# Kernel optimization log

Measured on AMD Instinct MI355X. Metric: run time of the kernel, lower is better.

## Reference

```python
import jax, jax.numpy as jnp
import numpy as np
from jax import lax

B, H, W = 256, 28, 28
LATENT = 64
SOM = (16, 16)
FLAT = 7 * 7 * 256  # encoder feature size after two 2x2 pools


def conv2d_same(x, w, b):
    # x: NHWC, w: HWIO
    return lax.conv_general_dilated(x, w, (1, 1), 'SAME',
                                    dimension_numbers=('NHWC', 'HWIO', 'NHWC')) + b


def maxpool_2x2(x):
    return lax.reduce_window(x, -jnp.inf, lax.max, (1, 2, 2, 1), (1, 2, 2, 1), 'SAME')


def upsample_2x(x):
    return jnp.repeat(jnp.repeat(x, 2, axis=1), 2, axis=2)


def encode(x, conv1_w, conv1_b, conv2_w, conv2_b, enc_w, enc_b):
    h = jax.nn.relu(conv2d_same(x, conv1_w, conv1_b))      # [B,28,28,256]
    h = maxpool_2x2(h)                                      # [B,14,14,256]
    h = jax.nn.relu(conv2d_same(h, conv2_w, conv2_b))      # [B,14,14,256]
    h = maxpool_2x2(h)                                      # [B,7,7,256]
    h = h.reshape(h.shape[0], -1)                           # [B,12544]
    return h @ enc_w + enc_b                                # [B,latent]


def decode(z, dec_w, dec_b, deconv1_w, deconv1_b, deconv2_w, deconv2_b):
    h = z @ dec_w + dec_b                                   # [B,12544]
    h = h.reshape(-1, 7, 7, 256)
    h = upsample_2x(h)                                      # [B,14,14,256]
    h = jax.nn.relu(conv2d_same(h, deconv1_w, deconv1_b))
    h = upsample_2x(h)                                      # [B,28,28,256]
    h = conv2d_same(h, deconv2_w, deconv2_b)                # [B,28,28,1]
    return jax.nn.sigmoid(h)


def setup_inputs() -> dict:
    key = jax.random.key(0)
    ks = jax.random.split(key, 12)
    tn = lambda k, shp, s: jax.random.truncated_normal(k, -2.0, 2.0, shp, jnp.float32) * s
    return {
        'x': jax.random.uniform(ks[0], (B, H, W, 1), jnp.float32),
        'conv1_w': tn(ks[1], (4, 4, 1, 256), 0.1),
        'conv1_b': jnp.full((256,), 0.1, jnp.float32),
        'conv2_w': tn(ks[2], (4, 4, 256, 256), 0.1),
        'conv2_b': jnp.full((256,), 0.1, jnp.float32),
        'enc_w': tn(ks[3], (FLAT, LATENT), 0.02),
        'enc_b': jnp.zeros((LATENT,), jnp.float32),
        'embeddings': tn(ks[4], (SOM[0], SOM[1], LATENT), 0.05),
        'dec_w': tn(ks[5], (LATENT, FLAT), 0.02),
        'dec_b': jnp.zeros((FLAT,), jnp.float32),
        'deconv1_w': tn(ks[6], (4, 4, 256, 256), 0.1),
        'deconv1_b': jnp.full((256,), 0.1, jnp.float32),
        'deconv2_w': tn(ks[7], (4, 4, 256, 1), 0.1),
        'deconv2_b': jnp.full((1,), 0.1, jnp.float32),
    }


def reference(x, conv1_w, conv1_b, conv2_w, conv2_b, enc_w, enc_b, embeddings,
              dec_w, dec_b, deconv1_w, deconv1_b, deconv2_w, deconv2_b):
    z_e = encode(x, conv1_w, conv1_b, conv2_w, conv2_b, enc_w, enc_b)  # [B,D]
    emb_flat = embeddings.reshape(-1, LATENT)                          # [K,D]
    # squared euclidean distances [B,K] (cdist pattern)
    z_dist_flat = jnp.sum(jnp.square(z_e[:, None, :] - emb_flat[None, :, :]), axis=-1)
    k = jnp.argmin(z_dist_flat, axis=-1)                               # [B]
    z_q = emb_flat[k]                                                  # [B,D]
    x_hat_e = decode(z_e, dec_w, dec_b, deconv1_w, deconv1_b, deconv2_w, deconv2_b)
    x_hat_q = decode(z_q, dec_w, dec_b, deconv1_w, deconv1_b, deconv2_w, deconv2_b)
    return jnp.stack([x_hat_e, x_hat_q], axis=0)  # [2,B,28,28,1]
```

## Files before the change

kernel.cpp:

```cpp
#include <hip/hip_runtime.h>
#include <hip/hip_bf16.h>

typedef unsigned short u16;
using short8 = __attribute__((ext_vector_type(8))) short;
using half8  = __attribute__((ext_vector_type(8))) _Float16;
using half4  = __attribute__((ext_vector_type(4))) _Float16;
using half2v = __attribute__((ext_vector_type(2))) _Float16;
using f32x4  = __attribute__((ext_vector_type(4))) float;

__device__ __forceinline__ u16 f2bf(float f) {
    unsigned int u = __float_as_uint(f);
    u += 0x7FFFu + ((u >> 16) & 1u);
    return (u16)(u >> 16);
}
__device__ __forceinline__ float bf2f(u16 h) {
    return __uint_as_float(((unsigned int)h) << 16);
}

__device__ __forceinline__ void gl_lds16(const void* g, void* l) {
    __builtin_amdgcn_global_load_lds((const __attribute__((address_space(1))) void*)g,
                                     (__attribute__((address_space(3))) void*)l, 16, 0, 0);
}

#define PIPE_WAIT8() asm volatile("s_waitcnt vmcnt(8)" ::: "memory")
#define PIPE_WAIT0() asm volatile("s_waitcnt vmcnt(0)" ::: "memory")
#define BAR() __builtin_amdgcn_s_barrier()

__global__ __launch_bounds__(256) void wprep_split_kernel(const float* __restrict__ src,
                                                          u16* __restrict__ hi, u16* __restrict__ lo) {
    int idx = blockIdx.x * 256 + threadIdx.x;
    int ci = idx & 255, n = (idx >> 8) & 255, kk = idx >> 16;
    float v = src[(kk * 256 + ci) * 256 + n];
    u16 h = f2bf(v);
    hi[idx] = h;
    lo[idx] = f2bf(v - bf2f(h));
}

__global__ __launch_bounds__(256) void wprep_dc1_par(const float* __restrict__ src, _Float16* __restrict__ dst) {
    const int idx = blockIdx.x * 256 + threadIdx.x;
    const int ci = idx & 255, n = (idx >> 8) & 255, tg = idx >> 16;
    int p, j;
    if (tg < 9)       { p = 0; j = tg; }
    else if (tg < 15) { p = 1; j = tg - 9; }
    else if (tg < 21) { p = 2; j = tg - 15; }
    else              { p = 3; j = tg - 21; }
    const int dy = p >> 1, dx = p & 1;
    const int nx = 3 - dx;
    const int oyi = j / nx, oxi = j % nx;
    int ky0, kyn, kx0, kxn;
    if (dy == 0) { ky0 = (oyi == 0) ? 0 : (oyi == 1 ? 1 : 3); kyn = (oyi == 1) ? 2 : 1; }
    else         { ky0 = (oyi == 0) ? 0 : 2;                  kyn = 2; }
    if (dx == 0) { kx0 = (oxi == 0) ? 0 : (oxi == 1 ? 1 : 3); kxn = (oxi == 1) ? 2 : 1; }
    else         { kx0 = (oxi == 0) ? 0 : 2;                  kxn = 2; }
    float s = 0.f;
    for (int a = 0; a < kyn; ++a)
        for (int c = 0; c < kxn; ++c)
            s += src[(((ky0 + a) * 4 + (kx0 + c)) * 256 + ci) * 256 + n];
    dst[((size_t)tg << 16) + (n << 8) + ci] = (_Float16)s;
}

__global__ __launch_bounds__(256) void wprep_dc2_par(const float* __restrict__ src, _Float16* __restrict__ dst) {
    const int idx = blockIdx.x * 256 + threadIdx.x;
    if (idx >= 9216) return;
    const int ci = idx & 255;
    const int j9 = (idx >> 8) % 9, p = (idx >> 8) / 9;
    const int dy = p >> 1, dx = p & 1;
    const int oyi = j9 / 3, oxi = j9 % 3;
    float s = 0.f;
    if (!((dy == 1 && oyi == 2) || (dx == 1 && oxi == 2))) {
        int ky0, kyn, kx0, kxn;
        if (dy == 0) { ky0 = (oyi == 0) ? 0 : (oyi == 1 ? 1 : 3); kyn = (oyi == 1) ? 2 : 1; }
        else         { ky0 = (oyi == 0) ? 0 : 2;                  kyn = 2; }
        if (dx == 0) { kx0 = (oxi == 0) ? 0 : (oxi == 1 ? 1 : 3); kxn = (oxi == 1) ? 2 : 1; }
        else         { kx0 = (oxi == 0) ? 0 : 2;                  kxn = 2; }
        for (int a = 0; a < kyn; ++a)
            for (int c = 0; c < kxn; ++c)
                s += src[((ky0 + a) * 4 + (kx0 + c)) * 256 + ci];
    }
    dst[idx] = (_Float16)s;
}

__global__ __launch_bounds__(256) void conv1_pool_v2(const float* __restrict__ x,
                                                     const float* __restrict__ w,
                                                     const float* __restrict__ bias,
                                                     u16* __restrict__ hi, u16* __restrict__ lo) {
    __shared__ float xs[5][32];
    const int blk = blockIdx.x;
    const int py = blk % 14, b = blk / 14;
    const int t = threadIdx.x;
    for (int i = t; i < 160; i += 256) {
        const int r = i >> 5, c = i & 31;
        const int gy = 2 * py - 1 + r, gx = c - 1;
        float v = 0.f;
        if ((unsigned)gy < 28u && (unsigned)gx < 28u) v = x[(b * 28 + gy) * 28 + gx];
        xs[r][c] = v;
    }
    __syncthreads();
    float wr[16];
#pragma unroll
    for (int k = 0; k < 16; ++k) wr[k] = w[k * 256 + t];
    const float bs = bias[t];
    for (int px = 0; px < 14; ++px) {
        float m = 0.f;
#pragma unroll
        for (int dy = 0; dy < 2; ++dy)
#pragma unroll
            for (int dx = 0; dx < 2; ++dx) {
                float a = bs;
#pragma unroll
                for (int ky = 0; ky < 4; ++ky)
#pragma unroll
                    for (int kx = 0; kx < 4; ++kx)
                        a += xs[dy + ky][2 * px + dx + kx] * wr[ky * 4 + kx];
                m = fmaxf(m, a);
            }
        u16 h = f2bf(m);
        const int o = ((b * 14 + py) * 14 + px) * 256 + t;
        hi[o] = h;
        lo[o] = f2bf(m - bf2f(h));
    }
}

__global__ __launch_bounds__(256, 2) void conv2_split_v3(const u16* __restrict__ Ih, const u16* __restrict__ Il,
                                                         const u16* __restrict__ Wh, const u16* __restrict__ Wl,
                                                         const u16* __restrict__ zg,
                                                         const float* __restrict__ bias, float* __restrict__ out) {
    __shared__ __align__(16) short lds[32768];
    const int t = threadIdx.x, lane = t & 63, w = t >> 6;
    const int wm = w >> 1, wn = w & 1;
    const int l16 = lane & 15, l4 = lane >> 4;
    const int m0 = blockIdx.x * 128, n0 = blockIdx.y * 128;

    const int rl8 = lane >> 3;
    const int g = (lane & 7) ^ rl8;
    const u16* selA = (g < 4 ? Ih : Il) + ((g & 3) << 3);
    const u16* selB = (g < 4 ? Wh : Wl) + ((g & 3) << 3);

    int ay[4], ax[4], ab[4], wb[4];
#pragma unroll
    for (int j = 0; j < 4; ++j) {
        const int r = w * 32 + j * 8 + rl8;
        const int gm = m0 + r;
        const int b = gm / 196, rem = gm % 196;
        ay[j] = rem / 14; ax[j] = rem % 14; ab[j] = b * 196;
        wb[j] = (n0 + r) << 8;
    }
    int aoff[4]; bool av[4];
    auto dectap = [&](int kk) {
        const int ky = kk >> 2, kx = kk & 3;
#pragma unroll
        for (int j = 0; j < 4; ++j) {
            const int iy = ay[j] + ky - 1, ix = ax[j] + kx - 1;
            av[j] = ((unsigned)iy < 14u) && ((unsigned)ix < 14u);
            aoff[j] = (ab[j] + iy * 14 + ix) << 8;
        }
    };
    int rdA[4], rdB[4];
#pragma unroll
    for (int mi = 0; mi < 4; ++mi) {
        const int ra = wm * 64 + mi * 16 + l16;
        rdA[mi] = (ra << 6) + ((l4 ^ (ra & 7)) << 3);
    }
#pragma unroll
    for (int ni = 0; ni < 4; ++ni) {
        const int rb = wn * 64 + ni * 16 + l16;
        rdB[ni] = 8192 + (rb << 6) + ((l4 ^ (rb & 7)) << 3);
    }
    auto stage = [&](int h) {
        const int kk = h >> 3, kc = (h & 7) << 5;
        const int buf = (h & 1) << 14;
#pragma unroll
        for (int j = 0; j < 4; ++j) {
            const int rowb = buf + ((w * 32 + j * 8) << 6);
            const u16* asrc = av[j] ? (selA + aoff[j] + kc) : zg;
            gl_lds16(asrc, lds + rowb);
            gl_lds16(selB + (kk << 16) + wb[j] + kc, lds + 8192 + rowb);
        }
    };

    f32x4 acc[4][4] = {};
    dectap(0);
    stage(0);
    for (int h = 0; h < 128; ++h) {
        const int hn = (h < 127) ? h + 1 : 127;
        if ((hn & 7) == 0) dectap(hn >> 3);
        stage(hn);
        PIPE_WAIT8();
        BAR();
        const int base = (h & 1) << 14;
        short8 bh8[4], bl8[4];
#pragma unroll
        for (int ni = 0; ni < 4; ++ni) {
            bh8[ni] = *(const short8*)&lds[base + rdB[ni]];
            bl8[ni] = *(const short8*)&lds[base + (rdB[ni] ^ 32)];
        }
#pragma unroll
        for (int mi = 0; mi < 4; ++mi) {
            const short8 ah = *(const short8*)&lds[base + rdA[mi]];
            const short8 al = *(const short8*)&lds[base + (rdA[mi] ^ 32)];
#pragma unroll
            for (int ni = 0; ni < 4; ++ni) {
                acc[mi][ni] = __builtin_amdgcn_mfma_f32_16x16x32_bf16(ah, bh8[ni], acc[mi][ni], 0, 0, 0);
                acc[mi][ni] = __builtin_amdgcn_mfma_f32_16x16x32_bf16(ah, bl8[ni], acc[mi][ni], 0, 0, 0);
                acc[mi][ni] = __builtin_amdgcn_mfma_f32_16x16x32_bf16(al, bh8[ni], acc[mi][ni], 0, 0, 0);
            }
        }
        BAR();
    }
    PIPE_WAIT0();
#pragma unroll
    for (int ni = 0; ni < 4; ++ni) {
        const int col = n0 + wn * 64 + ni * 16 + l16;
        const float bv = bias[col];
#pragma unroll
        for (int mi = 0; mi < 4; ++mi) {
            const int mrow = m0 + wm * 64 + mi * 16 + l4 * 4;
#pragma unroll
            for (int r = 0; r < 4; ++r)
                out[(size_t)(mrow + r) * 256 + col] = fmaxf(acc[mi][ni][r] + bv, 0.f);
        }
    }
}

__global__ __launch_bounds__(256, 2) void deconv1_par(const _Float16* __restrict__ I,
                                                      const _Float16* __restrict__ WC,
                                                      const _Float16* __restrict__ zg,
                                                      const float* __restrict__ bias,
                                                      _Float16* __restrict__ out) {
    __shared__ __align__(16) _Float16 lds[32768];
    const int t = threadIdx.x, lane = t & 63, w = t >> 6;
    const int wm = w >> 1, wn = w & 1;
    const int l16 = lane & 15, l4 = lane >> 4;
    const int m0 = blockIdx.x * 128, n0 = blockIdx.y * 128;
    const int p = blockIdx.z, dy = p >> 1, dx = p & 1;
    const int nx = 3 - dx;
    const int ntaps = (3 - dy) * nx;
    const int pbase = (dy == 0) ? (dx == 0 ? 0 : 9) : (dx == 0 ? 15 : 21);
    const int nkt = ntaps * 4;

    const int rl8 = lane >> 3;
    const int g = (lane & 7) ^ rl8;
    const _Float16* selA = I + (g << 3);
    const _Float16* selB = WC + ((size_t)pbase << 16) + (g << 3);

    int aY[4], aX[4], ab[4], wb[4];
#pragma unroll
    for (int j = 0; j < 4; ++j) {
        const int r = w * 32 + j * 8 + rl8;
        const int gm = m0 + r;
        const int b = gm / 49, rem = gm % 49;
        aY[j] = rem / 7; aX[j] = rem % 7; ab[j] = b * 49;
        wb[j] = (n0 + r) << 8;
    }
    int aoff[4]; bool av[4];
    auto dectap = [&](int kk) {
        const int oy = kk / nx - (dy == 0 ? 1 : 0);
        const int ox = kk % nx - (dx == 0 ? 1 : 0);
#pragma unroll
        for (int j = 0; j < 4; ++j) {
            const int iy = aY[j] + oy, ix = aX[j] + ox;
            av[j] = ((unsigned)iy < 7u) && ((unsigned)ix < 7u);
            aoff[j] = (ab[j] + iy * 7 + ix) << 8;
        }
    };
    int rdA[4], rdB[4];
#pragma unroll
    for (int mi = 0; mi < 4; ++mi) {
        const int ra = wm * 64 + mi * 16 + l16;
        rdA[mi] = (ra << 6) + ((l4 ^ (ra & 7)) << 3);
    }
#pragma unroll
    for (int ni = 0; ni < 4; ++ni) {
        const int rb = wn * 64 + ni * 16 + l16;
        rdB[ni] = 8192 + (rb << 6) + ((l4 ^ (rb & 7)) << 3);
    }
    auto stage = [&](int kt) {
        const int kk = kt >> 2, kc = (kt & 3) << 6;
        const int buf = (kt & 1) << 14;
#pragma unroll
        for (int j = 0; j < 4; ++j) {
            const int rowb = buf + ((w * 32 + j * 8) << 6);
            const _Float16* asrc = av[j] ? (selA + aoff[j] + kc) : zg;
            gl_lds16(asrc, lds + rowb);
            gl_lds16(selB + (kk << 16) + wb[j] + kc, lds + 8192 + rowb);
        }
    };

    f32x4 acc[4][4] = {};
    dectap(0);
    stage(0);
    for (int kt = 0; kt < nkt; ++kt) {
        const int ktn = (kt < nkt - 1) ? kt + 1 : kt;
        if ((ktn & 3) == 0 && ktn == kt + 1) dectap(ktn >> 2);
        stage(ktn);
        PIPE_WAIT8();
        BAR();
        const int base = (kt & 1) << 14;
#pragma unroll
        for (int ks = 0; ks < 2; ++ks) {
            const int x32 = ks << 5;
            half8 b8[4];
#pragma unroll
            for (int ni = 0; ni < 4; ++ni)
                b8[ni] = *(const half8*)&lds[base + (rdB[ni] ^ x32)];
#pragma unroll
            for (int mi = 0; mi < 4; ++mi) {
                const half8 a8 = *(const half8*)&lds[base + (rdA[mi] ^ x32)];
#pragma unroll
                for (int ni = 0; ni < 4; ++ni)
                    acc[mi][ni] = __builtin_amdgcn_mfma_f32_16x16x32_f16(a8, b8[ni], acc[mi][ni], 0, 0, 0);
            }
        }
        BAR();
    }
    PIPE_WAIT0();
#pragma unroll
    for (int mi = 0; mi < 4; ++mi) {
        const int mb = m0 + wm * 64 + mi * 16 + l4 * 4;
#pragma unroll
        for (int r = 0; r < 4; ++r) {
            const int m = mb + r;
            const int b = m / 49, rem = m % 49;
            const int Y = rem / 7, X = rem % 7;
            _Float16* op = out + (((size_t)(b * 196 + (2 * Y + dy) * 14 + (2 * X + dx))) << 8);
#pragma unroll
            for (int ni = 0; ni < 4; ++ni) {
                const int col = n0 + wn * 64 + ni * 16 + l16;
                op[col] = (_Float16)fmaxf(acc[mi][ni][r] + bias[col], 0.f);
            }
        }
    }
}

__global__ __launch_bounds__(256) void pool2_kernel(const float* __restrict__ h2, float* __restrict__ h2p) {
    int idx = blockIdx.x * 256 + threadIdx.x;
    int c = idx & 255;
    int rest = idx >> 8;
    int px = rest % 7, py = (rest / 7) % 7, b = rest / 49;
    const float* base = h2 + (((size_t)(b * 14 + 2 * py)) * 14 + 2 * px) * 256 + c;
    float v = fmaxf(fmaxf(base[0], base[256]), fmaxf(base[14 * 256], base[14 * 256 + 256]));
    h2p[idx] = v;
}

__global__ __launch_bounds__(256) void enc_kernel(const float* __restrict__ h2p, const float* __restrict__ ew,
                                                  const float* __restrict__ eb, float* __restrict__ zcat) {
    __shared__ float arow[12544];
    __shared__ float part[256];
    const int b = blockIdx.x, t = threadIdx.x;
    const float* src = h2p + (size_t)b * 12544;
    for (int i = t; i < 12544; i += 256) arow[i] = src[i];
    __syncthreads();
    const int n = t & 63, chunk = t >> 6;
    float acc = 0.f;
    const int k0 = chunk * 3136;
    for (int k = k0; k < k0 + 3136; ++k) acc += arow[k] * ew[k * 64 + n];
    part[t] = acc;
    __syncthreads();
    if (t < 64) zcat[b * 64 + t] = part[t] + part[t + 64] + part[t + 128] + part[t + 192] + eb[t];
}

__global__ __launch_bounds__(256) void som_kernel(const float* __restrict__ emb, float* __restrict__ zcat) {
    __shared__ float zrow[64];
    __shared__ float sd[256];
    __shared__ int si[256];
    const int b = blockIdx.x, t = threadIdx.x;
    if (t < 64) zrow[t] = zcat[b * 64 + t];
    __syncthreads();
    float acc = 0.f;
    const float* e = emb + t * 64;
    for (int d = 0; d < 64; ++d) { float df = zrow[d] - e[d]; acc += df * df; }
    sd[t] = acc; si[t] = t;
    __syncthreads();
    for (int off = 128; off >= 1; off >>= 1) {
        if (t < off) {
            float d2 = sd[t + off]; int i2 = si[t + off];
            if (d2 < sd[t] || (d2 == sd[t] && i2 < si[t])) { sd[t] = d2; si[t] = i2; }
        }
        __syncthreads();
    }
    const int k = si[0];
    if (t < 64) zcat[(256 + b) * 64 + t] = emb[k * 64 + t];
}

__global__ __launch_bounds__(256) void dec_kernel(const float* __restrict__ zcat, const float* __restrict__ dw,
                                                  const float* __restrict__ db, _Float16* __restrict__ dech) {
    __shared__ float z[8][64];
    const int t = threadIdx.x;
    const int bg = blockIdx.x / 49;
    const int nc = blockIdx.x % 49;
    for (int i = t; i < 512; i += 256) z[i >> 6][i & 63] = zcat[bg * 512 + i];
    __syncthreads();
    const int n = nc * 256 + t;
    const float bv = db[n];
    float acc[8];
#pragma unroll
    for (int j = 0; j < 8; ++j) acc[j] = bv;
    for (int k = 0; k < 64; ++k) {
        float wv = dw[(size_t)k * 12544 + n];
#pragma unroll
        for (int j = 0; j < 8; ++j) acc[j] += z[j][k] * wv;
    }
#pragma unroll
    for (int j = 0; j < 8; ++j) dech[((size_t)(bg * 8 + j)) * 12544 + n] = (_Float16)acc[j];
}

__global__ __launch_bounds__(256) void deconv2_v3(const _Float16* __restrict__ d1, const _Float16* __restrict__ w2c,
                                                  const float* __restrict__ bias, float* __restrict__ out) {
    __shared__ _Float16 ds[6400];
    __shared__ _Float16 wl[9216];
    const int t = threadIdx.x;
    const int blk = blockIdx.x;
    const int tile = blk % 49, b = blk / 49;
    const int ty = tile / 7, tx = tile % 7;
    const int iy0 = 2 * ty - 1, ix0 = 2 * tx - 1;
    for (int i = t; i < 2304; i += 256)
        *(half4*)&wl[i * 4] = *(const half4*)&w2c[i * 4];
    const half4 z4 = {};
    for (int i = t; i < 1600; i += 256) {
        const int pix = i >> 6, c4 = (i & 63) << 2;
        const int py = pix / 5, px = pix % 5;
        const int iy = iy0 + py, ix = ix0 + px;
        half4 v = z4;
        if ((unsigned)iy < 14u && (unsigned)ix < 14u)
            v = *(const half4*)&d1[(((size_t)(b * 14 + iy)) * 14 + ix) * 256 + c4];
        *(half4*)&ds[pix * 256 + c4] = v;
    }
    __syncthreads();
    const int wv = t >> 6, lane = t & 63;
    const int ci0 = lane * 4;
    const float bv = bias[0];
#pragma unroll
    for (int pp = 0; pp < 4; ++pp) {
        const int pq = wv + pp * 4;
        const int oy = ty * 4 + (pq >> 2), ox = tx * 4 + (pq & 3);
        const int dy = oy & 1, Y = oy >> 1;
        const int dxp = ox & 1, X = ox >> 1;
        const _Float16* wbase = wl + ((dy * 2 + dxp) * 9) * 256 + ci0;
        float acc = 0.f;
#pragma unroll
        for (int j = 0; j < 9; ++j) {
            const int oyi = j / 3, oxi = j % 3;
            const int iy = Y + oyi - (dy == 0 ? 1 : 0);
            const int ix = X + oxi - (dxp == 0 ? 1 : 0);
            const int lp = (iy - iy0) * 5 + (ix - ix0);
            const half4 dv = *(const half4*)&ds[lp * 256 + ci0];
            const half4 wv4 = *(const half4*)&wbase[j * 256];
            half2v dlo = {dv.x, dv.y}, dhi = {dv.z, dv.w};
            half2v wlo = {wv4.x, wv4.y}, whi = {wv4.z, wv4.w};
            acc = __builtin_amdgcn_fdot2(dlo, wlo, acc, false);
            acc = __builtin_amdgcn_fdot2(dhi, whi, acc, false);
        }
#pragma unroll
        for (int off = 32; off; off >>= 1) acc += __shfl_xor(acc, off);
        if (lane == 0) out[(size_t)b * 784 + oy * 28 + ox] = 1.f / (1.f + expf(-(acc + bv)));
    }
}

extern "C" void kernel_launch(void* const* d_in, const int* in_sizes, int n_in,
                              void* d_out, int out_size, void* d_ws, size_t ws_size,
                              hipStream_t stream) {
    const float* x    = (const float*)d_in[0];
    const float* c1w  = (const float*)d_in[1];
    const float* c1b  = (const float*)d_in[2];
    const float* c2w  = (const float*)d_in[3];
    const float* c2b  = (const float*)d_in[4];
    const float* ew   = (const float*)d_in[5];
    const float* eb   = (const float*)d_in[6];
    const float* emb  = (const float*)d_in[7];
    const float* dw   = (const float*)d_in[8];
    const float* db   = (const float*)d_in[9];
    const float* dc1w = (const float*)d_in[10];
    const float* dc1b = (const float*)d_in[11];
    const float* dc2w = (const float*)d_in[12];
    const float* dc2b = (const float*)d_in[13];
    float* out = (float*)d_out;

    char* ws = (char*)d_ws;
    size_t off = 0;
    auto alloc = [&](size_t bytes) { size_t o = off; off += (bytes + 255) & ~(size_t)255; return o; };

    u16*      h1p_hi = (u16*)(ws + alloc((size_t)256 * 196 * 256 * 2));
    u16*      h1p_lo = (u16*)(ws + alloc((size_t)256 * 196 * 256 * 2));
    u16*      w2T_hi = (u16*)(ws + alloc((size_t)16 * 256 * 256 * 2));
    u16*      w2T_lo = (u16*)(ws + alloc((size_t)16 * 256 * 256 * 2));
    float*    h2     = (float*)(ws + alloc((size_t)256 * 196 * 256 * 4));
    float*    h2p    = (float*)(ws + alloc((size_t)256 * 49 * 256 * 4));
    float*    zcat   = (float*)(ws + alloc((size_t)512 * 64 * 4));
    _Float16* dech   = (_Float16*)(ws + alloc((size_t)512 * 49 * 256 * 2));
    _Float16* wc1    = (_Float16*)(ws + alloc((size_t)25 * 256 * 256 * 2));
    _Float16* d1     = (_Float16*)(ws + alloc((size_t)512 * 196 * 256 * 2));
    _Float16* w2c    = (_Float16*)(ws + alloc((size_t)9216 * 2));
    u16*      zg     = (u16*)(ws + alloc(256));

    hipMemsetAsync(zg, 0, 256, stream);
    wprep_split_kernel<<<4096, 256, 0, stream>>>(c2w, w2T_hi, w2T_lo);
    wprep_dc1_par<<<6400, 256, 0, stream>>>(dc1w, wc1);
    wprep_dc2_par<<<36, 256, 0, stream>>>(dc2w, w2c);
    conv1_pool_v2<<<3584, 256, 0, stream>>>(x, c1w, c1b, h1p_hi, h1p_lo);
    conv2_split_v3<<<dim3(392, 2), 256, 0, stream>>>(h1p_hi, h1p_lo, w2T_hi, w2T_lo, zg, c2b, h2);
    pool2_kernel<<<12544, 256, 0, stream>>>(h2, h2p);
    enc_kernel<<<256, 256, 0, stream>>>(h2p, ew, eb, zcat);
    som_kernel<<<256, 256, 0, stream>>>(emb, zcat);
    dec_kernel<<<3136, 256, 0, stream>>>(zcat, dw, db, dech);
    deconv1_par<<<dim3(196, 2, 4), 256, 0, stream>>>(dech, wc1, (const _Float16*)zg, dc1b, d1);
    deconv2_v3<<<25088, 256, 0, stream>>>(d1, w2c, dc2b, out);
}
```

Before: 841.0 us.

## Switch conv GEMMs to 32x32 MFMA, split encoder matmul, retile deconv2

Conv2 and deconv1 move from 16x16x32 MFMA tiles to 32x32x16 tiles with 2x2 accumulators per wave. This cuts the number of LDS fragment reads per MFMA and changes the epilogue store pattern. The encoder dense layer becomes a split-K partial kernel over 98 chunks plus a reduction kernel, reusing the h2 buffer for the partials. Deconv2 now processes row bands per block, keeps its weights in registers and uses far fewer blocks, at the cost of more registers and a serial per-pixel loop.

```diff
diff --git a/kernel.cpp b/kernel.cpp
--- a/kernel.cpp
+++ b/kernel.cpp
@@ -7,6 +7,7 @@
 using half4  = __attribute__((ext_vector_type(4))) _Float16;
 using half2v = __attribute__((ext_vector_type(2))) _Float16;
 using f32x4  = __attribute__((ext_vector_type(4))) float;
+using f32x16 = __attribute__((ext_vector_type(16))) float;
 
 __device__ __forceinline__ u16 f2bf(float f) {
     unsigned int u = __float_as_uint(f);
@@ -121,14 +122,14 @@
     }
 }
 
-__global__ __launch_bounds__(256, 2) void conv2_split_v3(const u16* __restrict__ Ih, const u16* __restrict__ Il,
+__global__ __launch_bounds__(256, 2) void conv2_split_v4(const u16* __restrict__ Ih, const u16* __restrict__ Il,
                                                          const u16* __restrict__ Wh, const u16* __restrict__ Wl,
                                                          const u16* __restrict__ zg,
                                                          const float* __restrict__ bias, float* __restrict__ out) {
     __shared__ __align__(16) short lds[32768];
     const int t = threadIdx.x, lane = t & 63, w = t >> 6;
     const int wm = w >> 1, wn = w & 1;
-    const int l16 = lane & 15, l4 = lane >> 4;
+    const int l32 = lane & 31, lh = lane >> 5;
     const int m0 = blockIdx.x * 128, n0 = blockIdx.y * 128;
 
     const int rl8 = lane >> 3;
@@ -155,16 +156,24 @@
             aoff[j] = (ab[j] + iy * 14 + ix) << 8;
         }
     };
-    int rdA[4], rdB[4];
-#pragma unroll
-    for (int mi = 0; mi < 4; ++mi) {
-        const int ra = wm * 64 + mi * 16 + l16;
-        rdA[mi] = (ra << 6) + ((l4 ^ (ra & 7)) << 3);
-    }
-#pragma unroll
-    for (int ni = 0; ni < 4; ++ni) {
-        const int rb = wn * 64 + ni * 16 + l16;
-        rdB[ni] = 8192 + (rb << 6) + ((l4 ^ (rb & 7)) << 3);
+    int offA[2][2], offB[2][2];
+#pragma unroll
+    for (int mi = 0; mi < 2; ++mi) {
+        const int row = wm * 64 + mi * 32 + l32;
+#pragma unroll
+        for (int ks = 0; ks < 2; ++ks) {
+            const int c = ks * 2 + lh;
+            offA[mi][ks] = (row << 6) + ((c ^ (row & 7)) << 3);
+        }
+    }
+#pragma unroll
+    for (int ni = 0; ni < 2; ++ni) {
+        const int row = wn * 64 + ni * 32 + l32;
+#pragma unroll
+        for (int ks = 0; ks < 2; ++ks) {
+            const int c = ks * 2 + lh;
+            offB[ni][ks] = 8192 + (row << 6) + ((c ^ (row & 7)) << 3);
+        }
     }
     auto stage = [&](int h) {
         const int kk = h >> 3, kc = (h & 7) << 5;
@@ -178,59 +187,64 @@
         }
     };
 
-    f32x4 acc[4][4] = {};
+    f32x16 acc[2][2] = {};
     dectap(0);
     stage(0);
     for (int h = 0; h < 128; ++h) {
         const int hn = (h < 127) ? h + 1 : 127;
-        if ((hn & 7) == 0) dectap(hn >> 3);
+        if ((hn & 7) == 0 && hn == h + 1) dectap(hn >> 3);
         stage(hn);
         PIPE_WAIT8();
         BAR();
         const int base = (h & 1) << 14;
-        short8 bh8[4], bl8[4];
-#pragma unroll
-        for (int ni = 0; ni < 4; ++ni) {
-            bh8[ni] = *(const short8*)&lds[base + rdB[ni]];
-            bl8[ni] = *(const short8*)&lds[base + (rdB[ni] ^ 32)];
-        }
-#pragma unroll
-        for (int mi = 0; mi < 4; ++mi) {
-            const short8 ah = *(const short8*)&lds[base + rdA[mi]];
-            const short8 al = *(const short8*)&lds[base + (rdA[mi] ^ 32)];
-#pragma unroll
-            for (int ni = 0; ni < 4; ++ni) {
-                acc[mi][ni] = __builtin_amdgcn_mfma_f32_16x16x32_bf16(ah, bh8[ni], acc[mi][ni], 0, 0, 0);
-                acc[mi][ni] = __builtin_amdgcn_mfma_f32_16x16x32_bf16(ah, bl8[ni], acc[mi][ni], 0, 0, 0);
-                acc[mi][ni] = __builtin_amdgcn_mfma_f32_16x16x32_bf16(al, bh8[ni], acc[mi][ni], 0, 0, 0);
+#pragma unroll
+        for (int ks = 0; ks < 2; ++ks) {
+            short8 bh[2], bl[2];
+#pragma unroll
+            for (int ni = 0; ni < 2; ++ni) {
+                bh[ni] = *(const short8*)&lds[base + offB[ni][ks]];
+                bl[ni] = *(const short8*)&lds[base + (offB[ni][ks] ^ 32)];
+            }
+#pragma unroll
+            for (int mi = 0; mi < 2; ++mi) {
+                const short8 ah = *(const short8*)&lds[base + offA[mi][ks]];
+                const short8 al = *(const short8*)&lds[base + (offA[mi][ks] ^ 32)];
+#pragma unroll
+                for (int ni = 0; ni < 2; ++ni) {
+                    acc[mi][ni] = __builtin_amdgcn_mfma_f32_32x32x16_bf16(ah, bh[ni], acc[mi][ni], 0, 0, 0);
+                    acc[mi][ni] = __builtin_amdgcn_mfma_f32_32x32x16_bf16(ah, bl[ni], acc[mi][ni], 0, 0, 0);
+                    acc[mi][ni] = __builtin_amdgcn_mfma_f32_32x32x16_bf16(al, bh[ni], acc[mi][ni], 0, 0, 0);
+                }
             }
         }
         BAR();
     }
     PIPE_WAIT0();
 #pragma unroll
-    for (int ni = 0; ni < 4; ++ni) {
-        const int col = n0 + wn * 64 + ni * 16 + l16;
-        const float bv = bias[col];
-#pragma unroll
-        for (int mi = 0; mi < 4; ++mi) {
-            const int mrow = m0 + wm * 64 + mi * 16 + l4 * 4;
-#pragma unroll
-            for (int r = 0; r < 4; ++r)
-                out[(size_t)(mrow + r) * 256 + col] = fmaxf(acc[mi][ni][r] + bv, 0.f);
-        }
-    }
-}
-
-__global__ __launch_bounds__(256, 2) void deconv1_par(const _Float16* __restrict__ I,
-                                                      const _Float16* __restrict__ WC,
-                                                      const _Float16* __restrict__ zg,
-                                                      const float* __restrict__ bias,
-                                                      _Float16* __restrict__ out) {
+    for (int ni = 0; ni < 2; ++ni) {
+        const int n = n0 + wn * 64 + ni * 32 + l32;
+        const float bv = bias[n];
+#pragma unroll
+        for (int mi = 0; mi < 2; ++mi) {
+            const int mb = m0 + wm * 64 + mi * 32 + 4 * lh;
+#pragma unroll
+            for (int reg = 0; reg < 16; ++reg) {
+                const int m = mb + (reg & 3) + 8 * (reg >> 2);
+                out[(size_t)m * 256 + n] = fmaxf(acc[mi][ni][reg] + bv, 0.f);
+            }
+        }
+    }
+}
+
+__global__ __launch_bounds__(256, 2) void deconv1_par_v4(const _Float16* __restrict__ I,
+                                                         const _Float16* __restrict__ WC,
+                                                         const _Float16* __restrict__ zg,
+                                                         const float* __restrict__ bias,
+                                                         _Float16* __restrict__ out) {
     __shared__ __align__(16) _Float16 lds[32768];
     const int t = threadIdx.x, lane = t & 63, w = t >> 6;
     const int wm = w >> 1, wn = w & 1;
-    const int l16 = lane & 15, l4 = lane >> 4;
+    const int l32 = lane & 31, lh = lane >> 5;
     const int m0 = blockIdx.x * 128, n0 = blockIdx.y * 128;
     const int p = blockIdx.z, dy = p >> 1, dx = p & 1;
     const int nx = 3 - dx;
@@ -263,16 +277,24 @@
             aoff[j] = (ab[j] + iy * 7 + ix) << 8;
         }
     };
-    int rdA[4], rdB[4];
-#pragma unroll
-    for (int mi = 0; mi < 4; ++mi) {
-        const int ra = wm * 64 + mi * 16 + l16;
-        rdA[mi] = (ra << 6) + ((l4 ^ (ra & 7)) << 3);
-    }
-#pragma unroll
-    for (int ni = 0; ni < 4; ++ni) {
-        const int rb = wn * 64 + ni * 16 + l16;
-        rdB[ni] = 8192 + (rb << 6) + ((l4 ^ (rb & 7)) << 3);
+    int offA[2][4], offB[2][4];
+#pragma unroll
+    for (int mi = 0; mi < 2; ++mi) {
+        const int row = wm * 64 + mi * 32 + l32;
+#pragma unroll
+        for (int ks = 0; ks < 4; ++ks) {
+            const int c = ks * 2 + lh;
+            offA[mi][ks] = (row << 6) + ((c ^ (row & 7)) << 3);
+        }
+    }
+#pragma unroll
+    for (int ni = 0; ni < 2; ++ni) {
+        const int row = wn * 64 + ni * 32 + l32;
+#pragma unroll
+        for (int ks = 0; ks < 4; ++ks) {
+            const int c = ks * 2 + lh;
+            offB[ni][ks] = 8192 + (row << 6) + ((c ^ (row & 7)) << 3);
+        }
     }
     auto stage = [&](int kt) {
         const int kk = kt >> 2, kc = (kt & 3) << 6;
@@ -286,7 +308,7 @@
         }
     };
 
-    f32x4 acc[4][4] = {};
+    f32x16 acc[2][2] = {};
     dectap(0);
     stage(0);
     for (int kt = 0; kt < nkt; ++kt) {
@@ -297,36 +319,35 @@
         BAR();
         const int base = (kt & 1) << 14;
 #pragma unroll
-        for (int ks = 0; ks < 2; ++ks) {
-            const int x32 = ks << 5;
-            half8 b8[4];
-#pragma unroll
-            for (int ni = 0; ni < 4; ++ni)
-                b8[ni] = *(const half8*)&lds[base + (rdB[ni] ^ x32)];
-#pragma unroll
-            for (int mi = 0; mi < 4; ++mi) {
-                const half8 a8 = *(const half8*)&lds[base + (rdA[mi] ^ x32)];
-#pragma unroll
-                for (int ni = 0; ni < 4; ++ni)
-                    acc[mi][ni] = __builtin_amdgcn_mfma_f32_16x16x32_f16(a8, b8[ni], acc[mi][ni], 0, 0, 0);
+        for (int ks = 0; ks < 4; ++ks) {
+            half8 b8[2];
+#pragma unroll
+            for (int ni = 0; ni < 2; ++ni)
+                b8[ni] = *(const half8*)&lds[base + offB[ni][ks]];
+#pragma unroll
+            for (int mi = 0; mi < 2; ++mi) {
+                const half8 a8 = *(const half8*)&lds[base + offA[mi][ks]];
+#pragma unroll
+                for (int ni = 0; ni < 2; ++ni)
+                    acc[mi][ni] = __builtin_amdgcn_mfma_f32_32x32x16_f16(a8, b8[ni], acc[mi][ni], 0, 0, 0);
             }
         }
         BAR();
     }
     PIPE_WAIT0();
 #pragma unroll
-    for (int mi = 0; mi < 4; ++mi) {
-        const int mb = m0 + wm * 64 + mi * 16 + l4 * 4;
-#pragma unroll
-        for (int r = 0; r < 4; ++r) {
-            const int m = mb + r;
+    for (int mi = 0; mi < 2; ++mi) {
+        const int mb = m0 + wm * 64 + mi * 32 + 4 * lh;
+#pragma unroll
+        for (int reg = 0; reg < 16; ++reg) {
+            const int m = mb + (reg & 3) + 8 * (reg >> 2);
             const int b = m / 49, rem = m % 49;
             const int Y = rem / 7, X = rem % 7;
             _Float16* op = out + (((size_t)(b * 196 + (2 * Y + dy) * 14 + (2 * X + dx))) << 8);
 #pragma unroll
-            for (int ni = 0; ni < 4; ++ni) {
-                const int col = n0 + wn * 64 + ni * 16 + l16;
-                op[col] = (_Float16)fmaxf(acc[mi][ni][r] + bias[col], 0.f);
+            for (int ni = 0; ni < 2; ++ni) {
+                const int col = n0 + wn * 64 + ni * 32 + l32;
+                op[col] = (_Float16)fmaxf(acc[mi][ni][reg] + bias[col], 0.f);
             }
         }
     }
@@ -342,21 +363,38 @@
     h2p[idx] = v;
 }
 
-__global__ __launch_bounds__(256) void enc_kernel(const float* __restrict__ h2p, const float* __restrict__ ew,
-                                                  const float* __restrict__ eb, float* __restrict__ zcat) {
-    __shared__ float arow[12544];
-    __shared__ float part[256];
-    const int b = blockIdx.x, t = threadIdx.x;
-    const float* src = h2p + (size_t)b * 12544;
-    for (int i = t; i < 12544; i += 256) arow[i] = src[i];
-    __syncthreads();
-    const int n = t & 63, chunk = t >> 6;
-    float acc = 0.f;
-    const int k0 = chunk * 3136;
-    for (int k = k0; k < k0 + 3136; ++k) acc += arow[k] * ew[k * 64 + n];
-    part[t] = acc;
-    __syncthreads();
-    if (t < 64) zcat[b * 64 + t] = part[t] + part[t + 64] + part[t + 128] + part[t + 192] + eb[t];
+__global__ __launch_bounds__(256) void encp_kernel(const float* __restrict__ h2p, const float* __restrict__ ew,
+                                                   float* __restrict__ partials) {
+    __shared__ float ews[8192];
+    __shared__ float hbuf[8][128];
+    const int t = threadIdx.x, c = blockIdx.x;
+    const float* esrc = ew + (size_t)c * 8192;
+    for (int i = t; i < 2048; i += 256)
+        *(f32x4*)&ews[i * 4] = *(const f32x4*)&esrc[i * 4];
+    const int n = t & 63, sub = t >> 6;
+    const int rr = t >> 5, kq = (t & 31) << 2;
+    float* pout = partials + (size_t)c * 16384;
+    for (int bi = 0; bi < 32; ++bi) {
+        __syncthreads();
+        *(f32x4*)&hbuf[rr][kq] = *(const f32x4*)&h2p[(size_t)(bi * 8 + rr) * 12544 + c * 128 + kq];
+        __syncthreads();
+        float a0 = 0.f, a1 = 0.f;
+        for (int k = 0; k < 128; ++k) {
+            const float wv = ews[k * 64 + n];
+            a0 += hbuf[sub][k] * wv;
+            a1 += hbuf[sub + 4][k] * wv;
+        }
+        pout[(bi * 8 + sub) * 64 + n] = a0;
+        pout[(bi * 8 + sub + 4) * 64 + n] = a1;
+    }
+}
+
+__global__ __launch_bounds__(256) void encr_kernel(const float* __restrict__ partials, const float* __restrict__ eb,
+                                                   float* __restrict__ zcat) {
+    const int o = blockIdx.x * 256 + threadIdx.x;
+    float s = eb[o & 63];
+    for (int c = 0; c < 98; ++c) s += partials[(size_t)c * 16384 + o];
+    zcat[o] = s;
 }
 
 __global__ __launch_bounds__(256) void som_kernel(const float* __restrict__ emb, float* __restrict__ zcat) {
@@ -404,51 +442,47 @@
     for (int j = 0; j < 8; ++j) dech[((size_t)(bg * 8 + j)) * 12544 + n] = (_Float16)acc[j];
 }
 
-__global__ __launch_bounds__(256) void deconv2_v3(const _Float16* __restrict__ d1, const _Float16* __restrict__ w2c,
+__global__ __launch_bounds__(256) void deconv2_v5(const _Float16* __restrict__ d1, const _Float16* __restrict__ w2c,
                                                   const float* __restrict__ bias, float* __restrict__ out) {
-    __shared__ _Float16 ds[6400];
-    __shared__ _Float16 wl[9216];
+    __shared__ _Float16 ds[6 * 14 * 256];
     const int t = threadIdx.x;
     const int blk = blockIdx.x;
-    const int tile = blk % 49, b = blk / 49;
-    const int ty = tile / 7, tx = tile % 7;
-    const int iy0 = 2 * ty - 1, ix0 = 2 * tx - 1;
-    for (int i = t; i < 2304; i += 256)
-        *(half4*)&wl[i * 4] = *(const half4*)&w2c[i * 4];
-    const half4 z4 = {};
-    for (int i = t; i < 1600; i += 256) {
-        const int pix = i >> 6, c4 = (i & 63) << 2;
-        const int py = pix / 5, px = pix % 5;
-        const int iy = iy0 + py, ix = ix0 + px;
-        half4 v = z4;
-        if ((unsigned)iy < 14u && (unsigned)ix < 14u)
-            v = *(const half4*)&d1[(((size_t)(b * 14 + iy)) * 14 + ix) * 256 + c4];
-        *(half4*)&ds[pix * 256 + c4] = v;
-    }
+    const int q = blk & 3, b = blk >> 2;
+    const int r0 = (q == 3) ? 8 : 3 * q;
+    for (int i = t; i < 2688; i += 256) {
+        const int r = i / 448, rem = i % 448;
+        *(half8*)&ds[r * 3584 + rem * 8] =
+            *(const half8*)&d1[((size_t)(b * 14 + r0 + r) * 14) * 256 + rem * 8];
+    }
+    const int lane = t & 63, wv = t >> 6;
+    const int ch0 = lane * 4;
+    half4 wreg[4][9];
+#pragma unroll
+    for (int p = 0; p < 4; ++p)
+#pragma unroll
+        for (int j = 0; j < 9; ++j)
+            wreg[p][j] = *(const half4*)&w2c[(p * 9 + j) * 256 + ch0];
+    const float bv = bias[0];
     __syncthreads();
-    const int wv = t >> 6, lane = t & 63;
-    const int ci0 = lane * 4;
-    const float bv = bias[0];
-#pragma unroll
-    for (int pp = 0; pp < 4; ++pp) {
-        const int pq = wv + pp * 4;
-        const int oy = ty * 4 + (pq >> 2), ox = tx * 4 + (pq & 3);
+    for (int pi = 0; pi < 49; ++pi) {
+        const int ql = pi * 4 + wv;
+        const int oy = 7 * q + ql / 28, ox = ql % 28;
         const int dy = oy & 1, Y = oy >> 1;
         const int dxp = ox & 1, X = ox >> 1;
-        const _Float16* wbase = wl + ((dy * 2 + dxp) * 9) * 256 + ci0;
+        const half4* wp = wreg[dy * 2 + dxp];
         float acc = 0.f;
 #pragma unroll
         for (int j = 0; j < 9; ++j) {
-            const int oyi = j / 3, oxi = j % 3;
-            const int iy = Y + oyi - (dy == 0 ? 1 : 0);
-            const int ix = X + oxi - (dxp == 0 ? 1 : 0);
-            const int lp = (iy - iy0) * 5 + (ix - ix0);
-            const half4 dv = *(const half4*)&ds[lp * 256 + ci0];
-            const half4 wv4 = *(const half4*)&wbase[j * 256];
-            half2v dlo = {dv.x, dv.y}, dhi = {dv.z, dv.w};
-            half2v wlo = {wv4.x, wv4.y}, whi = {wv4.z, wv4.w};
-            acc = __builtin_amdgcn_fdot2(dlo, wlo, acc, false);
-            acc = __builtin_amdgcn_fdot2(dhi, whi, acc, false);
+            const int iy = Y + (j / 3) - (dy ? 0 : 1);
+            const int ix = X + (j % 3) - (dxp ? 0 : 1);
+            if (iy >= r0 && iy < r0 + 6 && (unsigned)ix < 14u) {
+                const half4 dv = *(const half4*)&ds[((iy - r0) * 14 + ix) * 256 + ch0];
+                const half4 w4 = wp[j];
+                half2v dlo = {dv.x, dv.y}, dhi = {dv.z, dv.w};
+                half2v wlo = {w4.x, w4.y}, whi = {w4.z, w4.w};
+                acc = __builtin_amdgcn_fdot2(dlo, wlo, acc, false);
+                acc = __builtin_amdgcn_fdot2(dhi, whi, acc, false);
+            }
         }
 #pragma unroll
         for (int off = 32; off; off >>= 1) acc += __shfl_xor(acc, off);
@@ -491,17 +525,19 @@
     _Float16* d1     = (_Float16*)(ws + alloc((size_t)512 * 196 * 256 * 2));
     _Float16* w2c    = (_Float16*)(ws + alloc((size_t)9216 * 2));
     u16*      zg     = (u16*)(ws + alloc(256));
+    float*    partials = h2;
 
     hipMemsetAsync(zg, 0, 256, stream);
     wprep_split_kernel<<<4096, 256, 0, stream>>>(c2w, w2T_hi, w2T_lo);
     wprep_dc1_par<<<6400, 256, 0, stream>>>(dc1w, wc1);
     wprep_dc2_par<<<36, 256, 0, stream>>>(dc2w, w2c);
     conv1_pool_v2<<<3584, 256, 0, stream>>>(x, c1w, c1b, h1p_hi, h1p_lo);
-    conv2_split_v3<<<dim3(392, 2), 256, 0, stream>>>(h1p_hi, h1p_lo, w2T_hi, w2T_lo, zg, c2b, h2);
+    conv2_split_v4<<<dim3(392, 2), 256, 0, stream>>>(h1p_hi, h1p_lo, w2T_hi, w2T_lo, zg, c2b, h2);
     pool2_kernel<<<12544, 256, 0, stream>>>(h2, h2p);
-    enc_kernel<<<256, 256, 0, stream>>>(h2p, ew, eb, zcat);
+    encp_kernel<<<98, 256, 0, stream>>>(h2p, ew, partials);
+    encr_kernel<<<64, 256, 0, stream>>>(partials, eb, zcat);
     som_kernel<<<256, 256, 0, stream>>>(emb, zcat);
     dec_kernel<<<3136, 256, 0, stream>>>(zcat, dw, db, dech);
-    deconv1_par<<<dim3(196, 2, 4), 256, 0, stream>>>(dech, wc1, (const _Float16*)zg, dc1b, d1);
-    deconv2_v3<<<25088, 256, 0, stream>>>(d1, w2c, dc2b, out);
-}
+    deconv1_par_v4<<<dim3(196, 2, 4), 256, 0, stream>>>(dech, wc1, (const _Float16*)zg, dc1b, d1);
+    deconv2_v5<<<2048, 256, 0, stream>>>(d1, w2c, dc2b, out);
+}
```

Result: slower. 1.084 ms (+28.8%).
